# Performance work log

Measured on AMD Instinct MI355X. Metric: run time of the kernel, lower is better.

## Reference

```python
import jax, jax.numpy as jnp
import numpy as np

B, S, D, H = 2, 2048, 1024, 16
DEPTH = D // H


def setup_inputs() -> dict:
    key = jax.random.key(0)
    ks = jax.random.split(key, 10)
    std = 1.0 / np.sqrt(D)
    v = jax.random.normal(ks[0], (B, S, D), jnp.float32)
    q = jax.random.normal(ks[1], (B, S, D), jnp.float32)
    k = jax.random.normal(ks[2], (B, S, D), jnp.float32)
    # padding mask: 1.0 at masked (padded) key positions, 0.0 elsewhere
    mask = (jax.random.uniform(ks[3], (B, 1, 1, S)) < 0.1).astype(jnp.float32)
    Wq = jax.random.normal(ks[4], (D, D), jnp.float32) * std
    bq = jnp.zeros((D,), jnp.float32)
    Wv = jax.random.normal(ks[5], (D, D), jnp.float32) * std
    bv = jnp.zeros((D,), jnp.float32)
    Wo = jax.random.normal(ks[6], (D, D), jnp.float32) * std
    bo = jnp.zeros((D,), jnp.float32)
    return {"v": v, "q": q, "k": k, "mask": mask,
            "Wq": Wq, "bq": bq, "Wv": Wv, "bv": bv, "Wo": Wo, "bo": bo}


def _split_heads(x):
    # (B, S, D) -> (B, H, S, depth)
    return x.reshape(B, S, H, DEPTH).transpose(0, 2, 1, 3)


def reference(v, q, k, mask, Wq, bq, Wv, bv, Wo, bo):
    # NOTE: faithful to source, keys are projected with the QUERY weights
    # (mixedK = self.wQuery(k) in the original code).
    Q = _split_heads(q @ Wq + bq)
    K = _split_heads(k @ Wq + bq)
    V = _split_heads(v @ Wv + bv)
    scale = 1.0 / jnp.sqrt(jnp.asarray(DEPTH, jnp.float32))
    logits = jnp.einsum('bhqd,bhkd->bhqk', Q, K) * scale
    logits = logits + mask * (-1e9)
    attn = jax.nn.softmax(logits, axis=-1)
    out = jnp.einsum('bhqk,bhkd->bhqd', attn, V)
    out = out.transpose(0, 2, 1, 3).reshape(B, S, D)
    return out @ Wo + bo
```

## Files before the change

kernel.cpp:

```cpp
#include <hip/hip_runtime.h>
#include <cstddef>


namespace {

constexpr int Ss = 2048;
constexpr int Dd = 1024;
constexpr int Mm = 4096;
constexpr int NT = Ss / 64;
constexpr float QSCALE = 0.18033688f;
constexpr float NEG2 = -1.442695041e9f;

typedef unsigned short u16;
typedef __attribute__((ext_vector_type(8))) __bf16 bf16x8;
typedef __attribute__((ext_vector_type(4))) float f32x4;
typedef __attribute__((ext_vector_type(16))) float f32x16;
typedef __attribute__((ext_vector_type(4))) unsigned int u32x4;
typedef __attribute__((ext_vector_type(2))) unsigned int u32x2;
typedef __attribute__((ext_vector_type(8))) unsigned short us8;

__device__ __forceinline__ u16 bfc(float f) {
  __bf16 h = (__bf16)f;
  return __builtin_bit_cast(u16, h);
}
__device__ __forceinline__ unsigned pack2(float lo, float hi) {
  return (unsigned)bfc(lo) | ((unsigned)bfc(hi) << 16);
}

__device__ __forceinline__ void gload_lds16(const void* g, void* l) {
  __builtin_amdgcn_global_load_lds(
      (__attribute__((address_space(1))) void*)g,
      (__attribute__((address_space(3))) void*)l, 16, 0, 0);
}

__device__ __forceinline__ f32x4 mfma16(bf16x8 a, bf16x8 b, f32x4 c) {
  return __builtin_amdgcn_mfma_f32_16x16x32_bf16(a, b, c, 0, 0, 0);
}
__device__ __forceinline__ f32x16 mfma32(bf16x8 a, bf16x8 b, f32x16 c) {
  return __builtin_amdgcn_mfma_f32_32x32x16_bf16(a, b, c, 0, 0, 0);
}
__device__ __forceinline__ float exp2_fast(float x) {
  return __builtin_amdgcn_exp2f(x);
}

__device__ __forceinline__ void pl32swap(unsigned& a, unsigned& b) {
#if __has_builtin(__builtin_amdgcn_permlane32_swap)
  u32x2 r = __builtin_amdgcn_permlane32_swap(a, b, false, false);
  a = r[0];
  b = r[1];
#else
  unsigned ax = (unsigned)__shfl_xor((int)a, 32);
  unsigned bx = (unsigned)__shfl_xor((int)b, 32);
  bool hi = (threadIdx.x & 63) >= 32;
  unsigned na = hi ? bx : a;
  unsigned nb = hi ? b : ax;
  a = na;
  b = nb;
#endif
}

__device__ __forceinline__ int swz(int row, int col) {
  return row * 64 + ((((col >> 3) ^ (row & 7)) << 3) | (col & 7));
}
__device__ __forceinline__ int src_col(int lane) {
  return ((lane & 7) ^ (lane >> 3)) * 8;
}

__global__ __launch_bounds__(256) void wt_transpose(const float* __restrict__ W0,
                                                    const float* __restrict__ W1,
                                                    const float* __restrict__ W2,
                                                    u16* __restrict__ wsbase) {
  const float* W = (blockIdx.z == 0) ? W0 : (blockIdx.z == 1) ? W1 : W2;
  u16* WT = wsbase + (size_t)blockIdx.z * (1024 * 1024);
  __shared__ float tile[32][33];
  const int tid = threadIdx.x;
  const int tx = tid & 31;
  const int ty = tid >> 5;
  const int n0 = blockIdx.x * 32;
  const int k0 = blockIdx.y * 32;
#pragma unroll
  for (int i = 0; i < 4; ++i)
    tile[ty + i * 8][tx] = W[(size_t)(k0 + ty + i * 8) * 1024 + n0 + tx];
  __syncthreads();
  const int r = tid >> 3;
  const int c4 = (tid & 7) * 4;
  ushort4 o4 = make_ushort4(bfc(tile[c4 + 0][r]), bfc(tile[c4 + 1][r]),
                            bfc(tile[c4 + 2][r]), bfc(tile[c4 + 3][r]));
  *(ushort4*)(&WT[(size_t)(n0 + r) * 1024 + k0 + c4]) = o4;
}

__global__ __launch_bounds__(256) void cvt_bf16(const float* __restrict__ q,
                                                const float* __restrict__ k,
                                                const float* __restrict__ v,
                                                u16* __restrict__ qb,
                                                u16* __restrict__ kb,
                                                u16* __restrict__ vb) {
  const int which = (int)(blockIdx.x >> 11);
  const int blk = (int)(blockIdx.x & 2047);
  const float* src = (which == 0) ? q : (which == 1) ? k : v;
  u16* dst = (which == 0) ? qb : (which == 1) ? kb : vb;
  const int base = (blk * 256 + (int)threadIdx.x) * 8;
  const float4 a = *(const float4*)(src + base);
  const float4 b = *(const float4*)(src + base + 4);
  us8 o;
  o[0] = bfc(a.x); o[1] = bfc(a.y); o[2] = bfc(a.z); o[3] = bfc(a.w);
  o[4] = bfc(b.x); o[5] = bfc(b.y); o[6] = bfc(b.z); o[7] = bfc(b.w);
  *(us8*)(dst + base) = o;
}

__global__ __launch_bounds__(256) void proj_qkv(
    const u16* __restrict__ qb, const u16* __restrict__ kb,
    const u16* __restrict__ vb, const u16* __restrict__ WqT,
    const u16* __restrict__ WvT, const float* __restrict__ bq,
    const float* __restrict__ bv, u16* __restrict__ Qp, u16* __restrict__ Kp,
    u16* __restrict__ VpT) {
  constexpr int K = 1024, N = 1024, M = 4096;
  __shared__ u16 As[128 * 64];
  __shared__ u16 Bs[128 * 64];
  const int lin = (int)blockIdx.x;
  const int xcd = lin & 7;
  const int j = lin >> 3;
  const int panel = xcd * 12 + (j >> 3);
  const int ntile = j & 7;
  const int z = panel >> 5;
  const int mtile = panel & 31;
  const int n0 = ntile * 128;
  const int m0 = mtile * 128;

  const u16* A = (z == 0) ? qb : (z == 1) ? kb : vb;
  const u16* Bt = (z == 2) ? WvT : WqT;
  const float* bias = (z == 2) ? bv : bq;
  const float cscale = (z == 0) ? QSCALE : 1.0f;

  const int tid = threadIdx.x;
  const int wid = tid >> 6;
  const int lane = tid & 63;
  const int g = lane >> 4;
  const int lr = lane & 15;
  const int wr = wid >> 1, wc = wid & 1;

  const f32x4 zero = {0.f, 0.f, 0.f, 0.f};
  f32x4 acc[4][4];
#pragma unroll
  for (int m = 0; m < 4; ++m)
#pragma unroll
    for (int n = 0; n < 4; ++n) acc[m][n] = zero;

  for (int kt = 0; kt < 16; ++kt) {
#pragma unroll
    for (int jj = 0; jj < 4; ++jj) {
      int rb = (wid * 4 + jj) * 8;
      gload_lds16(&A[(size_t)(m0 + rb + (lane >> 3)) * K + kt * 64 + src_col(lane)],
                  &As[rb * 64]);
      gload_lds16(&Bt[(size_t)(n0 + rb + (lane >> 3)) * K + kt * 64 + src_col(lane)],
                  &Bs[rb * 64]);
    }
    __syncthreads();
#pragma unroll
    for (int kk = 0; kk < 2; ++kk) {
      bf16x8 a[4], b[4];
#pragma unroll
      for (int m = 0; m < 4; ++m)
        a[m] = *(const bf16x8*)(&As[swz(wr * 64 + m * 16 + lr, kk * 32 + g * 8)]);
#pragma unroll
      for (int n = 0; n < 4; ++n)
        b[n] = *(const bf16x8*)(&Bs[swz(wc * 64 + n * 16 + lr, kk * 32 + g * 8)]);
#pragma unroll
      for (int m = 0; m < 4; ++m)
#pragma unroll
        for (int n = 0; n < 4; ++n) acc[m][n] = mfma16(a[m], b[n], acc[m][n]);
    }
    __syncthreads();
  }

#pragma unroll
  for (int n = 0; n < 4; ++n) {
    const int col = n0 + wc * 64 + n * 16 + lr;
    const float bv_ = bias[col];
#pragma unroll
    for (int m = 0; m < 4; ++m) {
      const int rowb = m0 + wr * 64 + m * 16 + g * 4;
      if (z == 2) {
        ushort4 o4 = make_ushort4(bfc(acc[m][n][0] + bv_), bfc(acc[m][n][1] + bv_),
                                  bfc(acc[m][n][2] + bv_), bfc(acc[m][n][3] + bv_));
        *(ushort4*)(&VpT[(size_t)col * M + rowb]) = o4;
      } else {
        u16* Cp = (z == 0) ? Qp : Kp;
#pragma unroll
        for (int r = 0; r < 4; ++r)
          Cp[(size_t)(rowb + r) * N + col] = bfc((acc[m][n][r] + bv_) * cscale);
      }
    }
  }
}

__global__ __launch_bounds__(256) void gemm_o(const u16* __restrict__ Ap,
                                              const u16* __restrict__ Bt,
                                              const float* __restrict__ bias,
                                              float* __restrict__ Cp) {
  constexpr int K = 1024, N = 1024;
  __shared__ u16 As[128 * 64];
  __shared__ u16 Bs[64 * 64];
  const int lin = (int)blockIdx.x;
  const int xcd = lin & 7;
  const int j = lin >> 3;
  const int mtile = xcd * 4 + (j >> 4);
  const int ntile = j & 15;
  const int n0 = ntile * 64;
  const int m0 = mtile * 128;

  const int tid = threadIdx.x;
  const int wid = tid >> 6;
  const int lane = tid & 63;
  const int g = lane >> 4;
  const int lr = lane & 15;

  const f32x4 zero = {0.f, 0.f, 0.f, 0.f};
  f32x4 acc[2][4];
#pragma unroll
  for (int m = 0; m < 2; ++m)
#pragma unroll
    for (int n = 0; n < 4; ++n) acc[m][n] = zero;

  for (int k0 = 0; k0 < K; k0 += 64) {
#pragma unroll
    for (int jj = 0; jj < 4; ++jj) {
      int rb = (wid * 4 + jj) * 8;
      gload_lds16(&Ap[(size_t)(m0 + rb + (lane >> 3)) * K + k0 + src_col(lane)],
                  &As[rb * 64]);
    }
#pragma unroll
    for (int jj = 0; jj < 2; ++jj) {
      int rb = (wid * 2 + jj) * 8;
      gload_lds16(&Bt[(size_t)(n0 + rb + (lane >> 3)) * K + k0 + src_col(lane)],
                  &Bs[rb * 64]);
    }
    __syncthreads();
#pragma unroll
    for (int kk = 0; kk < 2; ++kk) {
      bf16x8 a[2], b[4];
#pragma unroll
      for (int m = 0; m < 2; ++m)
        a[m] = *(const bf16x8*)(&As[swz(wid * 32 + m * 16 + lr, kk * 32 + g * 8)]);
#pragma unroll
      for (int n = 0; n < 4; ++n)
        b[n] = *(const bf16x8*)(&Bs[swz(n * 16 + lr, kk * 32 + g * 8)]);
#pragma unroll
      for (int m = 0; m < 2; ++m)
#pragma unroll
        for (int n = 0; n < 4; ++n) acc[m][n] = mfma16(a[m], b[n], acc[m][n]);
    }
    __syncthreads();
  }
#pragma unroll
  for (int n = 0; n < 4; ++n) {
    const int col = n0 + n * 16 + lr;
    const float bv_ = bias[col];
#pragma unroll
    for (int m = 0; m < 2; ++m) {
      const int rowb = m0 + wid * 32 + m * 16 + g * 4;
#pragma unroll
      for (int r = 0; r < 4; ++r)
        Cp[(size_t)(rowb + r) * N + col] = acc[m][n][r] + bv_;
    }
  }
}

__global__ __launch_bounds__(256) void attn32(const u16* __restrict__ Qp,
                                              const u16* __restrict__ Kp,
                                              const u16* __restrict__ VpT,
                                              const float* __restrict__ mask,
                                              u16* __restrict__ Op) {
  __shared__ u16 Ks[2][64 * 64];
  __shared__ u16 Vt[2][64 * 64];
  __shared__ float ms[2][64];
  __shared__ float redbuf[4][32];
  const int tid = threadIdx.x;
  const int wid = tid >> 6;
  const int lane = tid & 63;
  const int l31 = lane & 31;
  const int hi = lane >> 5;
  const int lin = (int)(blockIdx.x + (blockIdx.y << 4));
  const int wl = (lin & 7) * 64 + (lin >> 3);
  const int qt = wl & 15;
  const int bh = wl >> 4;
  const int b = bh >> 4;
  const int h = bh & 15;
  const int q0 = qt * 128;
  const size_t base = ((size_t)b * Ss) * Dd + (size_t)h * 64;
  const size_t vbase = (size_t)h * 64 * Mm + (size_t)b * Ss;
  const int qrow = q0 + wid * 32 + l31;

  bf16x8 qf[4];
#pragma unroll
  for (int ks = 0; ks < 4; ++ks)
    qf[ks] = *(const bf16x8*)(&Qp[base + (size_t)qrow * Dd + ks * 16 + hi * 8]);

  f32x16 oacc[2];
#pragma unroll
  for (int i = 0; i < 2; ++i)
#pragma unroll
    for (int r = 0; r < 16; ++r) oacc[i][r] = 0.f;
  float mrun = -1e30f, lrun = 0.f;

  auto stageKV = [&](int t, int buf) {
    const int key0 = t * 64;
#pragma unroll
    for (int jj = 0; jj < 2; ++jj) {
      int rb = (wid * 2 + jj) * 8;
      gload_lds16(&Kp[base + (size_t)(key0 + rb + (lane >> 3)) * Dd + src_col(lane)],
                  &Ks[buf][rb * 64]);
      gload_lds16(&VpT[vbase + (size_t)(rb + (lane >> 3)) * Mm + key0 + src_col(lane)],
                  &Vt[buf][rb * 64]);
    }
  };

  stageKV(0, 0);
  float msr = 0.f;
  if (tid < 64) ms[0][tid] = mask[(size_t)b * Ss + tid] * NEG2;
  __syncthreads();

  int cur = 0;
  for (int t = 0; t < NT; ++t) {
    const bool more = (t + 1) < NT;
    if (more) {
      stageKV(t + 1, cur ^ 1);
      if (tid < 64) msr = mask[(size_t)b * Ss + (t + 1) * 64 + tid];
    }
    f32x16 sacc[2];
#pragma unroll
    for (int sub = 0; sub < 2; ++sub)
#pragma unroll
      for (int a = 0; a < 4; ++a) {
        const f32x4 mv = *(const f32x4*)(&ms[cur][sub * 32 + a * 8 + hi * 4]);
#pragma unroll
        for (int jj = 0; jj < 4; ++jj) sacc[sub][a * 4 + jj] = mv[jj];
      }
    __builtin_amdgcn_s_setprio(1);
#pragma unroll
    for (int sub = 0; sub < 2; ++sub)
#pragma unroll
      for (int ks = 0; ks < 4; ++ks) {
        bf16x8 kf =
            *(const bf16x8*)(&Ks[cur][swz(sub * 32 + l31, ks * 16 + hi * 8)]);
        sacc[sub] = mfma32(kf, qf[ks], sacc[sub]);
      }
    __builtin_amdgcn_s_setprio(0);

    float mx[16];
#pragma unroll
    for (int r = 0; r < 16; ++r) mx[r] = fmaxf(sacc[0][r], sacc[1][r]);
#pragma unroll
    for (int s = 8; s >= 1; s >>= 1)
#pragma unroll
      for (int r = 0; r < s; ++r) mx[r] = fmaxf(mx[r], mx[r + s]);
    float rm = fmaxf(mx[0], __shfl_xor(mx[0], 32));

    if (__any(rm > mrun + 10.0f)) {
      const float mnew = fmaxf(mrun, rm);
      const float corr = exp2_fast(mrun - mnew);
      lrun *= corr;
      mrun = mnew;
      redbuf[wid][l31] = corr;
      f32x4 cv[4];
#pragma unroll
      for (int a = 0; a < 4; ++a)
        cv[a] = *(const f32x4*)(&redbuf[wid][a * 8 + hi * 4]);
#pragma unroll
      for (int d = 0; d < 2; ++d)
#pragma unroll
        for (int r = 0; r < 16; ++r) oacc[d][r] *= cv[r >> 2][r & 3];
    }
    float sm[16];
#pragma unroll
    for (int sub = 0; sub < 2; ++sub)
#pragma unroll
      for (int r = 0; r < 16; ++r) sacc[sub][r] = exp2_fast(sacc[sub][r] - mrun);
#pragma unroll
    for (int r = 0; r < 16; ++r) sm[r] = sacc[0][r] + sacc[1][r];
#pragma unroll
    for (int s = 8; s >= 1; s >>= 1)
#pragma unroll
      for (int r = 0; r < s; ++r) sm[r] += sm[r + s];
    lrun += sm[0] + __shfl_xor(sm[0], 32);

    bf16x8 pa[4];
#pragma unroll
    for (int sub = 0; sub < 2; ++sub)
#pragma unroll
      for (int half = 0; half < 2; ++half) {
        const int bse = half * 8;
        unsigned A0 = pack2(sacc[sub][bse + 0], sacc[sub][bse + 1]);
        unsigned A1 = pack2(sacc[sub][bse + 2], sacc[sub][bse + 3]);
        unsigned B0 = pack2(sacc[sub][bse + 4], sacc[sub][bse + 5]);
        unsigned B1 = pack2(sacc[sub][bse + 6], sacc[sub][bse + 7]);
        pl32swap(A0, B0);
        pl32swap(A1, B1);
        u32x4 w = {A0, A1, B0, B1};
        pa[sub * 2 + half] = __builtin_bit_cast(bf16x8, w);
      }

    __builtin_amdgcn_s_setprio(1);
#pragma unroll
    for (int dsub = 0; dsub < 2; ++dsub)
#pragma unroll
      for (int ks = 0; ks < 4; ++ks) {
        bf16x8 vf =
            *(const bf16x8*)(&Vt[cur][swz(dsub * 32 + l31, ks * 16 + hi * 8)]);
        oacc[dsub] = mfma32(pa[ks], vf, oacc[dsub]);
      }
    __builtin_amdgcn_s_setprio(0);

    if (more && tid < 64) ms[cur ^ 1][tid] = msr * NEG2;
    __syncthreads();
    cur ^= 1;
  }

  redbuf[wid][l31] = 1.0f / lrun;
  f32x4 cv[4];
#pragma unroll
  for (int a = 0; a < 4; ++a)
    cv[a] = *(const f32x4*)(&redbuf[wid][a * 8 + hi * 4]);
#pragma unroll
  for (int dsub = 0; dsub < 2; ++dsub) {
    const int col = h * 64 + dsub * 32 + l31;
#pragma unroll
    for (int r = 0; r < 16; ++r) {
      const int row = q0 + wid * 32 + (r & 3) + 8 * (r >> 2) + 4 * hi;
      Op[((size_t)b * Ss + row) * Dd + col] = bfc(oacc[dsub][r] * cv[r >> 2][r & 3]);
    }
  }
}

}

extern "C" void kernel_launch(void* const* d_in, const int* in_sizes, int n_in,
                              void* d_out, int out_size, void* d_ws, size_t ws_size,
                              hipStream_t stream) {
  (void)in_sizes; (void)n_in; (void)out_size; (void)ws_size;
  const float* v = (const float*)d_in[0];
  const float* q = (const float*)d_in[1];
  const float* k = (const float*)d_in[2];
  const float* mask = (const float*)d_in[3];
  const float* Wq = (const float*)d_in[4];
  const float* bq = (const float*)d_in[5];
  const float* Wv = (const float*)d_in[6];
  const float* bv = (const float*)d_in[7];
  const float* Wo = (const float*)d_in[8];
  const float* bo = (const float*)d_in[9];
  float* out = (float*)d_out;

  constexpr size_t MEG = 1024 * 1024;
  u16* ws = (u16*)d_ws;
  u16* WqT = ws;
  u16* WvT = ws + 1 * MEG;
  u16* WoT = ws + 2 * MEG;
  u16* qb  = ws + 3 * MEG;
  u16* kb  = ws + 7 * MEG;
  u16* vb  = ws + 11 * MEG;
  u16* Qp  = ws + 15 * MEG;
  u16* Kp  = ws + 19 * MEG;
  u16* VpT = ws + 23 * MEG;
  u16* AO  = qb;

  wt_transpose<<<dim3(32, 32, 3), 256, 0, stream>>>(Wq, Wv, Wo, ws);
  cvt_bf16<<<dim3(6144), 256, 0, stream>>>(q, k, v, qb, kb, vb);
  proj_qkv<<<dim3(768), 256, 0, stream>>>(qb, kb, vb, WqT, WvT, bq, bv, Qp, Kp, VpT);
  attn32<<<dim3(16, 32), 256, 0, stream>>>(Qp, Kp, VpT, mask, AO);
  gemm_o<<<dim3(512), 256, 0, stream>>>(AO, WoT, bo, out);
}
```

Before: 143.9 us.

## Triple-buffer LDS tiles with single vmcnt-gated barrier in gemm_o and attention

Both the output-projection GEMM and the attention kernel move from double-buffered (or single-buffered) LDS staging with two __syncthreads per iteration to a three-stage ring. Loads are issued two tiles ahead, and each iteration starts with one s_waitcnt vmcnt plus barrier. The attention kernel also preloads the whole mask row into LDS once instead of streaming 64 entries per tile. This is meant to hide global-load latency and halve barrier count, at the cost of more LDS per block, which may reduce occupancy.

```diff
diff --git a/kernel.cpp b/kernel.cpp
--- a/kernel.cpp
+++ b/kernel.cpp
@@ -58,6 +58,14 @@
   b = nb;
 #endif
 }
+
+#define PIPE_BARRIER_V(N)                                  \
+  do {                                                     \
+    asm volatile("s_waitcnt vmcnt(" #N ")" ::: "memory");  \
+    __builtin_amdgcn_sched_barrier(0);                     \
+    __builtin_amdgcn_s_barrier();                          \
+    __builtin_amdgcn_sched_barrier(0);                     \
+  } while (0)
 
 __device__ __forceinline__ int swz(int row, int col) {
   return row * 64 + ((((col >> 3) ^ (row & 7)) << 3) | (col & 7));
@@ -199,8 +207,8 @@
                                               const float* __restrict__ bias,
                                               float* __restrict__ Cp) {
   constexpr int K = 1024, N = 1024;
-  __shared__ u16 As[128 * 64];
-  __shared__ u16 Bs[64 * 64];
+  __shared__ u16 As[3][128 * 64];
+  __shared__ u16 Bs[3][64 * 64];
   const int lin = (int)blockIdx.x;
   const int xcd = lin & 7;
   const int j = lin >> 3;
@@ -222,35 +230,49 @@
 #pragma unroll
     for (int n = 0; n < 4; ++n) acc[m][n] = zero;
 
-  for (int k0 = 0; k0 < K; k0 += 64) {
+  auto stage = [&](int kt, u16* as, u16* bs) {
 #pragma unroll
     for (int jj = 0; jj < 4; ++jj) {
       int rb = (wid * 4 + jj) * 8;
-      gload_lds16(&Ap[(size_t)(m0 + rb + (lane >> 3)) * K + k0 + src_col(lane)],
-                  &As[rb * 64]);
+      gload_lds16(&Ap[(size_t)(m0 + rb + (lane >> 3)) * K + kt * 64 + src_col(lane)],
+                  as + rb * 64);
     }
 #pragma unroll
     for (int jj = 0; jj < 2; ++jj) {
       int rb = (wid * 2 + jj) * 8;
-      gload_lds16(&Bt[(size_t)(n0 + rb + (lane >> 3)) * K + k0 + src_col(lane)],
-                  &Bs[rb * 64]);
-    }
-    __syncthreads();
+      gload_lds16(&Bt[(size_t)(n0 + rb + (lane >> 3)) * K + kt * 64 + src_col(lane)],
+                  bs + rb * 64);
+    }
+  };
+
+  stage(0, As[0], Bs[0]);
+  stage(1, As[1], Bs[1]);
+
+  int b0 = 0;
+  for (int kt = 0; kt < 16; ++kt) {
+    if (kt < 15) PIPE_BARRIER_V(6);
+    else         PIPE_BARRIER_V(0);
+    if (kt + 2 < 16) {
+      int b2 = b0 + 2; if (b2 >= 3) b2 -= 3;
+      stage(kt + 2, As[b2], Bs[b2]);
+    }
+    const u16* as = As[b0];
+    const u16* bs = Bs[b0];
 #pragma unroll
     for (int kk = 0; kk < 2; ++kk) {
       bf16x8 a[2], b[4];
 #pragma unroll
       for (int m = 0; m < 2; ++m)
-        a[m] = *(const bf16x8*)(&As[swz(wid * 32 + m * 16 + lr, kk * 32 + g * 8)]);
+        a[m] = *(const bf16x8*)(&as[swz(wid * 32 + m * 16 + lr, kk * 32 + g * 8)]);
 #pragma unroll
       for (int n = 0; n < 4; ++n)
-        b[n] = *(const bf16x8*)(&Bs[swz(n * 16 + lr, kk * 32 + g * 8)]);
+        b[n] = *(const bf16x8*)(&bs[swz(n * 16 + lr, kk * 32 + g * 8)]);
 #pragma unroll
       for (int m = 0; m < 2; ++m)
 #pragma unroll
         for (int n = 0; n < 4; ++n) acc[m][n] = mfma16(a[m], b[n], acc[m][n]);
     }
-    __syncthreads();
+    b0 = (b0 == 2) ? 0 : b0 + 1;
   }
 #pragma unroll
   for (int n = 0; n < 4; ++n) {
@@ -271,9 +293,9 @@
                                               const u16* __restrict__ VpT,
                                               const float* __restrict__ mask,
                                               u16* __restrict__ Op) {
-  __shared__ u16 Ks[2][64 * 64];
-  __shared__ u16 Vt[2][64 * 64];
-  __shared__ float ms[2][64];
+  __shared__ u16 Ks[3][64 * 64];
+  __shared__ u16 Vt[3][64 * 64];
+  __shared__ float msall[Ss];
   __shared__ float redbuf[4][32];
   const int tid = threadIdx.x;
   const int wid = tid >> 6;
@@ -291,48 +313,64 @@
   const size_t vbase = (size_t)h * 64 * Mm + (size_t)b * Ss;
   const int qrow = q0 + wid * 32 + l31;
 
-  bf16x8 qf[4];
-#pragma unroll
-  for (int ks = 0; ks < 4; ++ks)
-    qf[ks] = *(const bf16x8*)(&Qp[base + (size_t)qrow * Dd + ks * 16 + hi * 8]);
-
-  f32x16 oacc[2];
-#pragma unroll
-  for (int i = 0; i < 2; ++i)
-#pragma unroll
-    for (int r = 0; r < 16; ++r) oacc[i][r] = 0.f;
-  float mrun = -1e30f, lrun = 0.f;
-
-  auto stageKV = [&](int t, int buf) {
+  auto stageKV = [&](int t, u16* ksb, u16* vtb) {
     const int key0 = t * 64;
 #pragma unroll
     for (int jj = 0; jj < 2; ++jj) {
       int rb = (wid * 2 + jj) * 8;
       gload_lds16(&Kp[base + (size_t)(key0 + rb + (lane >> 3)) * Dd + src_col(lane)],
-                  &Ks[buf][rb * 64]);
+                  ksb + rb * 64);
       gload_lds16(&VpT[vbase + (size_t)(rb + (lane >> 3)) * Mm + key0 + src_col(lane)],
-                  &Vt[buf][rb * 64]);
+                  vtb + rb * 64);
     }
   };
 
-  stageKV(0, 0);
-  float msr = 0.f;
-  if (tid < 64) ms[0][tid] = mask[(size_t)b * Ss + tid] * NEG2;
-  __syncthreads();
-
-  int cur = 0;
+  bf16x8 qf[4];
+#pragma unroll
+  for (int ks = 0; ks < 4; ++ks)
+    qf[ks] = *(const bf16x8*)(&Qp[base + (size_t)qrow * Dd + ks * 16 + hi * 8]);
+  const float4 mk0 = *(const float4*)(&mask[(size_t)b * Ss + tid * 8]);
+  const float4 mk1 = *(const float4*)(&mask[(size_t)b * Ss + tid * 8 + 4]);
+
+  stageKV(0, Ks[0], Vt[0]);
+  stageKV(1, Ks[1], Vt[1]);
+
+  {
+    f32x4 s0 = {mk0.x * NEG2, mk0.y * NEG2, mk0.z * NEG2, mk0.w * NEG2};
+    f32x4 s1 = {mk1.x * NEG2, mk1.y * NEG2, mk1.z * NEG2, mk1.w * NEG2};
+    *(f32x4*)(&msall[tid * 8]) = s0;
+    *(f32x4*)(&msall[tid * 8 + 4]) = s1;
+  }
+  asm volatile("s_waitcnt lgkmcnt(0)" ::: "memory");
+  __builtin_amdgcn_sched_barrier(0);
+  __builtin_amdgcn_s_barrier();
+  __builtin_amdgcn_sched_barrier(0);
+
+  f32x16 oacc[2];
+#pragma unroll
+  for (int i = 0; i < 2; ++i)
+#pragma unroll
+    for (int r = 0; r < 16; ++r) oacc[i][r] = 0.f;
+  float mrun = -1e30f, lrun = 0.f;
+
+  int b0 = 0;
   for (int t = 0; t < NT; ++t) {
-    const bool more = (t + 1) < NT;
-    if (more) {
-      stageKV(t + 1, cur ^ 1);
-      if (tid < 64) msr = mask[(size_t)b * Ss + (t + 1) * 64 + tid];
-    }
+    if (t < NT - 1) PIPE_BARRIER_V(4);
+    else            PIPE_BARRIER_V(0);
+    if (t + 2 < NT) {
+      int b2 = b0 + 2; if (b2 >= 3) b2 -= 3;
+      stageKV(t + 2, Ks[b2], Vt[b2]);
+    }
+    const u16* ks = Ks[b0];
+    const u16* vt = Vt[b0];
+    const float* msp = &msall[t * 64];
+
     f32x16 sacc[2];
 #pragma unroll
     for (int sub = 0; sub < 2; ++sub)
 #pragma unroll
       for (int a = 0; a < 4; ++a) {
-        const f32x4 mv = *(const f32x4*)(&ms[cur][sub * 32 + a * 8 + hi * 4]);
+        const f32x4 mv = *(const f32x4*)(&msp[sub * 32 + a * 8 + hi * 4]);
 #pragma unroll
         for (int jj = 0; jj < 4; ++jj) sacc[sub][a * 4 + jj] = mv[jj];
       }
@@ -340,10 +378,10 @@
 #pragma unroll
     for (int sub = 0; sub < 2; ++sub)
 #pragma unroll
-      for (int ks = 0; ks < 4; ++ks) {
+      for (int ks_ = 0; ks_ < 4; ++ks_) {
         bf16x8 kf =
-            *(const bf16x8*)(&Ks[cur][swz(sub * 32 + l31, ks * 16 + hi * 8)]);
-        sacc[sub] = mfma32(kf, qf[ks], sacc[sub]);
+            *(const bf16x8*)(&ks[swz(sub * 32 + l31, ks_ * 16 + hi * 8)]);
+        sacc[sub] = mfma32(kf, qf[ks_], sacc[sub]);
       }
     __builtin_amdgcn_s_setprio(0);
 
@@ -404,16 +442,14 @@
 #pragma unroll
     for (int dsub = 0; dsub < 2; ++dsub)
 #pragma unroll
-      for (int ks = 0; ks < 4; ++ks) {
+      for (int ks_ = 0; ks_ < 4; ++ks_) {
         bf16x8 vf =
-            *(const bf16x8*)(&Vt[cur][swz(dsub * 32 + l31, ks * 16 + hi * 8)]);
-        oacc[dsub] = mfma32(pa[ks], vf, oacc[dsub]);
+            *(const bf16x8*)(&vt[swz(dsub * 32 + l31, ks_ * 16 + hi * 8)]);
+        oacc[dsub] = mfma32(pa[ks_], vf, oacc[dsub]);
       }
     __builtin_amdgcn_s_setprio(0);
 
-    if (more && tid < 64) ms[cur ^ 1][tid] = msr * NEG2;
-    __syncthreads();
-    cur ^= 1;
+    b0 = (b0 == 2) ? 0 : b0 + 1;
   }
 
   redbuf[wid][l31] = 1.0f / lrun;
```

After: 141.9 us. Within noise of the previous version (-1.4%).
